# Kernel tuning notes

Hardware: AMD Instinct MI355X
Metric: run time of the kernel (lower is better)

## Reference

```python
import jax, jax.numpy as jnp
import numpy as np

N = 100000   # skill_num
D = 128      # skill_embed_dim
E = 500000   # edges per relation
S = 16384    # queried skills
NEG_SLOPE = 0.2


def _gat(x, edge_index, W, att_src, att_dst, bias):
    # PyG GATConv, heads=1, add_self_loops=True, eval mode (no dropout)
    n = x.shape[0]
    loops = jnp.arange(n)
    src = jnp.concatenate([edge_index[0], loops])
    dst = jnp.concatenate([edge_index[1], loops])
    h = x @ W                              # [N, D]
    a_src = h @ att_src                    # [N]
    a_dst = h @ att_dst                    # [N]
    e = jax.nn.leaky_relu(a_src[src] + a_dst[dst], NEG_SLOPE)  # [E+N]
    emax = jax.ops.segment_max(e, dst, num_segments=n)
    ex = jnp.exp(e - emax[dst])
    denom = jax.ops.segment_sum(ex, dst, num_segments=n)
    alpha = ex / (denom[dst] + 1e-16)
    out = jax.ops.segment_sum(alpha[:, None] * h[src], dst, num_segments=n)
    return out + bias


def _sage(x, edge_index, Wl, bl, Wr):
    # PyG SAGEConv, aggr='mean', root_weight=True (lin_r has no bias)
    n = x.shape[0]
    src, dst = edge_index[0], edge_index[1]
    ones = jnp.ones((src.shape[0],), dtype=x.dtype)
    deg = jax.ops.segment_sum(ones, dst, num_segments=n)
    agg = jax.ops.segment_sum(x[src], dst, num_segments=n)
    agg = agg / jnp.maximum(deg, 1.0)[:, None]
    return agg @ Wl + bl + x @ Wr


def setup_inputs() -> dict:
    key = jax.random.key(0)
    ks = jax.random.split(key, 16)
    sc = 1.0 / np.sqrt(D)
    inp = {
        "s": jax.random.randint(ks[0], (S,), 0, N),
        "t_s": 0,
        "t_e": 12,
        "ei_parent": jax.random.randint(ks[1], (2, E), 0, N),
        "ei_child": jax.random.randint(ks[2], (2, E), 0, N),
        "ei_relate": jax.random.randint(ks[3], (2, E), 0, N),
        "emb": jax.random.normal(ks[4], (N, D), dtype=jnp.float32),
        # GAT is_parent params
        "Wp": jax.random.normal(ks[5], (D, D), dtype=jnp.float32) * sc,
        "asp": jax.random.normal(ks[6], (D,), dtype=jnp.float32) * sc,
        "adp": jax.random.normal(ks[7], (D,), dtype=jnp.float32) * sc,
        "bp": jnp.zeros((D,), dtype=jnp.float32),
        # GAT is_child params
        "Wc": jax.random.normal(ks[8], (D, D), dtype=jnp.float32) * sc,
        "asc": jax.random.normal(ks[9], (D,), dtype=jnp.float32) * sc,
        "adc": jax.random.normal(ks[10], (D,), dtype=jnp.float32) * sc,
        "bc": jnp.zeros((D,), dtype=jnp.float32),
        # SAGE relate params
        "Wl": jax.random.normal(ks[11], (D, D), dtype=jnp.float32) * sc,
        "bl": jnp.zeros((D,), dtype=jnp.float32),
        "Wr": jax.random.normal(ks[12], (D, D), dtype=jnp.float32) * sc,
    }
    return inp


def reference(s, t_s, t_e, ei_parent, ei_child, ei_relate, emb,
              Wp, asp, adp, bp, Wc, asc, adc, bc, Wl, bl, Wr):
    out_parent = _gat(emb, ei_parent, Wp, asp, adp, bp)
    out_child = _gat(emb, ei_child, Wc, asc, adc, bc)
    out_relate = _sage(emb, ei_relate, Wl, bl, Wr)
    # HeteroConv(aggr='mean') over the three relation outputs
    node_out = (out_parent + out_child + out_relate) / 3.0
    return node_out[s, :]
```

## Files before the change

kernel.cpp:

```cpp
#include <hip/hip_runtime.h>

#define D 128
#define CAP 64
#define OVF_CAP 1024

typedef short bf16x8 __attribute__((ext_vector_type(8)));
typedef float f32x4 __attribute__((ext_vector_type(4)));

__device__ __forceinline__ unsigned short f2bf(float f) {
  unsigned u = __builtin_bit_cast(unsigned, f);
  unsigned r = (u + 0x7fffu + ((u >> 16) & 1u)) >> 16;
  return (unsigned short)r;
}
__device__ __forceinline__ float bflo(unsigned r) {
  return __builtin_bit_cast(float, r << 16);
}
__device__ __forceinline__ float bfhi(unsigned r) {
  return __builtin_bit_cast(float, r & 0xffff0000u);
}
__device__ __forceinline__ float lrelu(float t) {
  return t >= 0.f ? t : 0.2f * t;
}
__device__ __forceinline__ int swz(int b) { return b ^ (((b >> 8) & 7) << 4); }


__global__ void k_setup(const float* __restrict__ Wp, const float* __restrict__ asp,
                        const float* __restrict__ adp, const float* __restrict__ Wc,
                        const float* __restrict__ asc, const float* __restrict__ adc,
                        const float* __restrict__ bp, const float* __restrict__ bc,
                        const float* __restrict__ bl, const float* __restrict__ Wl,
                        const float* __restrict__ Wr,
                        float* __restrict__ v, unsigned short* __restrict__ wpack,
                        int* __restrict__ qid, int* __restrict__ counters,
                        int* __restrict__ deg5, int N, int S5) {
  int i = blockIdx.x * blockDim.x + threadIdx.x;
  int stride = gridDim.x * blockDim.x;
  for (int k = i; k < N; k += stride) qid[k] = -1;
  for (int k = i; k < S5; k += stride) deg5[k] = 0;
  if (i < 16) counters[i] = 0;

  for (int idx = i; idx < 16 * 8 * 64 * 8; idx += stride) {
    int j    = idx & 7;
    int lane = (idx >> 3) & 63;
    int nt   = (idx >> 9) & 7;
    int kt   = idx >> 12;
    int o = kt >> 2;
    int c = (kt & 3) * 32 + (lane >> 4) * 8 + j;
    int n = nt * 16 + (lane & 15);
    const float* W = (o == 0) ? Wp : (o == 1) ? Wc : (o == 2) ? Wl : Wr;
    wpack[idx] = f2bf(W[c * D + n]);
  }

  if (blockIdx.x == 0 && threadIdx.x < 128) {
    int k = threadIdx.x;
    float s0 = 0.f, s1 = 0.f, s2 = 0.f, s3 = 0.f;
    for (int d = 0; d < D; ++d) {
      float wp = Wp[k * D + d], wc = Wc[k * D + d];
      s0 += wp * asp[d]; s1 += wp * adp[d];
      s2 += wc * asc[d]; s3 += wc * adc[d];
    }
    v[k] = s0; v[D + k] = s1; v[2 * D + k] = s2; v[3 * D + k] = s3;
    v[4 * D + k] = bp[k] + bc[k] + bl[k];
  }
}

__global__ void k_pre(const int* __restrict__ s, int* __restrict__ qid,
                      int* __restrict__ uniq, int* __restrict__ counters, int S,
                      const float* __restrict__ emb, const float* __restrict__ v,
                      float* __restrict__ a_sp, float* __restrict__ a_dp,
                      float* __restrict__ a_sc, float* __restrict__ a_dc,
                      float* __restrict__ selfP, float* __restrict__ selfC,
                      unsigned* __restrict__ ebf, int N) {
  int gtid = blockIdx.x * blockDim.x + threadIdx.x;
  int lane = threadIdx.x & 63;
  if (gtid < S) {
    int n = s[gtid];
    bool won = (atomicCAS(&qid[n], -1, -2) == -1);
    unsigned long long mask = __ballot(won);
    if (mask != 0ull) {
      int leader = __builtin_ctzll(mask);
      int base = 0;
      if (lane == leader) base = atomicAdd(&counters[0], __popcll(mask));
      base = __shfl(base, leader);
      if (won) {
        int u = base + __popcll(mask & ((1ull << lane) - 1ull));
        uniq[u] = n;
        qid[n] = u;
      }
    }
  }
  int node = (gtid >> 6) * 2 + (lane >> 5);
  int c = lane & 31;
  if (node >= N) return;
  float4 x4 = ((const float4*)(emb + (size_t)node * D))[c];
  uint2 p;
  p.x = ((unsigned)f2bf(x4.x)) | (((unsigned)f2bf(x4.y)) << 16);
  p.y = ((unsigned)f2bf(x4.z)) | (((unsigned)f2bf(x4.w)) << 16);
  ((uint2*)ebf)[(size_t)node * 32 + c] = p;
  float4 v0 = ((const float4*)(v))[c];
  float4 v1 = ((const float4*)(v + D))[c];
  float4 v2 = ((const float4*)(v + 2 * D))[c];
  float4 v3 = ((const float4*)(v + 3 * D))[c];
  float s0 = x4.x * v0.x + x4.y * v0.y + x4.z * v0.z + x4.w * v0.w;
  float s1 = x4.x * v1.x + x4.y * v1.y + x4.z * v1.z + x4.w * v1.w;
  float s2 = x4.x * v2.x + x4.y * v2.y + x4.z * v2.z + x4.w * v2.w;
  float s3 = x4.x * v3.x + x4.y * v3.y + x4.z * v3.z + x4.w * v3.w;
#pragma unroll
  for (int o = 16; o > 0; o >>= 1) {
    s0 += __shfl_down(s0, o);
    s1 += __shfl_down(s1, o);
    s2 += __shfl_down(s2, o);
    s3 += __shfl_down(s3, o);
  }
  if (c == 0) {
    a_sp[node] = s0; a_dp[node] = s1; a_sc[node] = s2; a_dc[node] = s3;
    selfP[node] = __expf(lrelu(s0 + s1));
    selfC[node] = __expf(lrelu(s2 + s3));
  }
}

__global__ void __launch_bounds__(256) k_filter(
    const int* __restrict__ eiP, const int* __restrict__ eiC,
    const int* __restrict__ eiR, const int* __restrict__ qid,
    int2* __restrict__ bktP, int2* __restrict__ bktC, int* __restrict__ bktR,
    int* __restrict__ degP, int* __restrict__ degC, int* __restrict__ degR,
    float* __restrict__ denP, float* __restrict__ denC,
    const float* __restrict__ a_sp, const float* __restrict__ a_dp,
    const float* __restrict__ a_sc, const float* __restrict__ a_dc,
    int2* __restrict__ ovf, int* __restrict__ counters, int E) {
  int rel = blockIdx.y;
  const int* ei = (rel == 0) ? eiP : (rel == 1) ? eiC : eiR;
  int e = blockIdx.x * 256 + threadIdx.x;
  if (e >= E) return;
  int dst = ei[E + e];
  int u = qid[dst];
  if (u < 0) return;
  int src = ei[e];
  int* deg = (rel == 0) ? degP : (rel == 1) ? degC : degR;
  int pos = atomicAdd(&deg[u], 1);
  if (rel == 2) {
    if (pos < CAP) {
      bktR[u * CAP + pos] = src;
    } else {
      int o = atomicAdd(&counters[6], 1);
      if (o < OVF_CAP) { int2 tt; tt.x = src; tt.y = u; ovf[2 * OVF_CAP + o] = tt; }
    }
  } else {
    const float* a_s = (rel == 0) ? a_sp : a_sc;
    const float* a_d = (rel == 0) ? a_dp : a_dc;
    float wgt = __expf(lrelu(a_s[src] + a_d[dst]));
    atomicAdd((rel == 0) ? &denP[u] : &denC[u], wgt);
    if (pos < CAP) {
      int2 tt; tt.x = src; tt.y = __builtin_bit_cast(int, wgt);
      ((rel == 0) ? bktP : bktC)[u * CAP + pos] = tt;
    } else {
      int o = atomicAdd(&counters[4 + rel], 1);
      if (o < OVF_CAP) { int2 tt; tt.x = src; tt.y = u; ovf[rel * OVF_CAP + o] = tt; }
    }
  }
}

__global__ void __launch_bounds__(512, 4) k_fused(
    const int2* __restrict__ bktP, const int2* __restrict__ bktC,
    const int* __restrict__ bktR,
    const int* __restrict__ degP, const int* __restrict__ degC,
    const int* __restrict__ degR,
    const float* __restrict__ denP, const float* __restrict__ denC,
    const float* __restrict__ a_sp, const float* __restrict__ a_dp,
    const float* __restrict__ a_sc, const float* __restrict__ a_dc,
    const float* __restrict__ selfP, const float* __restrict__ selfC,
    const unsigned* __restrict__ ebf, const float* __restrict__ emb,
    const int* __restrict__ uniq, const int* __restrict__ counters,
    const int2* __restrict__ ovf, const float* __restrict__ vvec,
    const unsigned short* __restrict__ wpack, float* __restrict__ outU) {
  __shared__ __align__(16) unsigned short A_lds[16 * 64 * 8];
  int U = counters[0];
  int u0 = blockIdx.x * 16;
  if (u0 >= U) return;
  int tid = threadIdx.x;
  int w = tid >> 6;
  int lane = tid & 63;

  int Lc[3];
#pragma unroll
  for (int r = 0; r < 3; ++r) {
    int L = counters[4 + r];
    Lc[r] = (L > OVF_CAP) ? OVF_CAP : L;
  }

#pragma unroll
  for (int t = 0; t < 2; ++t) {
    int m = 2 * w + t;
    int u = u0 + m;
    float2 z[4];
    if (u < U) {
      int n = uniq[u];
      float2 x2 = ((const float2*)(emb + (size_t)n * D))[lane];
#pragma unroll
      for (int r = 0; r < 3; ++r) {
        int dg = ((r == 0) ? degP : (r == 1) ? degC : degR)[u];
        int mc = (dg < CAP) ? dg : CAP;
        int srcl = 0;
        float wl = 0.f;
        if (r < 2) {
          if (lane < mc) {
            int2 sw_ = ((r == 0) ? bktP : bktC)[u * CAP + lane];
            srcl = sw_.x;
            wl = __builtin_bit_cast(float, sw_.y);
          }
        } else {
          if (lane < mc) { srcl = bktR[u * CAP + lane]; wl = 1.f; }
        }
        float2 a; a.x = 0.f; a.y = 0.f;
        int i = 0;
        for (; i + 4 <= mc; i += 4) {
          int s0 = __shfl(srcl, i),     s1 = __shfl(srcl, i + 1);
          int s2 = __shfl(srcl, i + 2), s3 = __shfl(srcl, i + 3);
          float w0 = __shfl(wl, i),     w1 = __shfl(wl, i + 1);
          float w2 = __shfl(wl, i + 2), w3 = __shfl(wl, i + 3);
          unsigned r0 = ebf[(size_t)s0 * 64 + lane];
          unsigned r1 = ebf[(size_t)s1 * 64 + lane];
          unsigned r2 = ebf[(size_t)s2 * 64 + lane];
          unsigned r3 = ebf[(size_t)s3 * 64 + lane];
          a.x += w0 * bflo(r0) + w1 * bflo(r1) + w2 * bflo(r2) + w3 * bflo(r3);
          a.y += w0 * bfhi(r0) + w1 * bfhi(r1) + w2 * bfhi(r2) + w3 * bfhi(r3);
        }
        for (; i < mc; ++i) {
          int si = __shfl(srcl, i);
          float wi = __shfl(wl, i);
          unsigned rr = ebf[(size_t)si * 64 + lane];
          a.x += wi * bflo(rr);
          a.y += wi * bfhi(rr);
        }
        if (dg > CAP) {
          const float* a_s = (r == 0) ? a_sp : a_sc;
          float adn = (r == 0) ? a_dp[n] : (r == 1) ? a_dc[n] : 0.f;
          for (int l = 0; l < Lc[r]; ++l) {
            int2 ov = ovf[r * OVF_CAP + l];
            if (ov.y == u) {
              float wv = 1.f;
              if (r < 2) wv = __expf(lrelu(a_s[ov.x] + adn));
              unsigned rr = ebf[(size_t)ov.x * 64 + lane];
              a.x += wv * bflo(rr);
              a.y += wv * bfhi(rr);
            }
          }
        }
        if (r == 2) {
          float dgc = (float)dg; if (dgc < 1.f) dgc = 1.f;
          float rc = 1.f / dgc;
          a.x *= rc; a.y *= rc;
        }
        z[r] = a;
      }
      float wP = selfP[n];
      float rP = 1.f / (denP[u] + wP);
      float wC = selfC[n];
      float rC = 1.f / (denC[u] + wC);
      z[0].x = (z[0].x + wP * x2.x) * rP; z[0].y = (z[0].y + wP * x2.y) * rP;
      z[1].x = (z[1].x + wC * x2.x) * rC; z[1].y = (z[1].y + wC * x2.y) * rC;
      z[3] = x2;
    } else {
      z[0].x = 0.f; z[0].y = 0.f; z[1] = z[0]; z[2] = z[0]; z[3] = z[0];
    }
    int ktc = lane >> 4;
    int q = (lane >> 2) & 3;
    int j0 = 2 * (lane & 3);
#pragma unroll
    for (int o = 0; o < 4; ++o) {
      int kt = o * 4 + ktc;
      unsigned pk = ((unsigned)f2bf(z[o].x)) | (((unsigned)f2bf(z[o].y)) << 16);
      int off = ((kt * 64 + q * 16 + m) * 8 + j0) * 2;
      *(unsigned*)((char*)A_lds + swz(off)) = pk;
    }
  }
  __syncthreads();

  f32x4 acc = {0.f, 0.f, 0.f, 0.f};
  const bf16x8* wp = (const bf16x8*)wpack;
#pragma unroll
  for (int kt = 0; kt < 16; ++kt) {
    bf16x8 a = *(const bf16x8*)((const char*)A_lds + swz((kt * 64 + lane) * 16));
    bf16x8 b = wp[(kt * 8 + w) * 64 + lane];
    acc = __builtin_amdgcn_mfma_f32_16x16x32_bf16(a, b, acc, 0, 0, 0);
  }

  int col = w * 16 + (lane & 15);
  int r0 = (lane >> 4) * 4;
  float bv = vvec[4 * D + col] * (1.f / 3.f);
#pragma unroll
  for (int reg = 0; reg < 4; ++reg) {
    int u = u0 + r0 + reg;
    if (u < U) outU[(size_t)u * D + col] = acc[reg] * (1.f / 3.f) + bv;
  }
}

__global__ void k_gather(const int* __restrict__ s, const int* __restrict__ qid,
                         const float* __restrict__ outU, float* __restrict__ out, int S) {
  int idx = blockIdx.x * blockDim.x + threadIdx.x;
  if (idx >= S * D) return;
  int i = idx >> 7;
  int d = idx & (D - 1);
  int u = qid[s[i]];
  out[idx] = outU[(size_t)u * D + d];
}


extern "C" void kernel_launch(void* const* d_in, const int* in_sizes, int n_in,
                              void* d_out, int out_size, void* d_ws, size_t ws_size,
                              hipStream_t stream) {
  const int*   s   = (const int*)d_in[0];
  const int*   eip = (const int*)d_in[3];
  const int*   eic = (const int*)d_in[4];
  const int*   eir = (const int*)d_in[5];
  const float* emb = (const float*)d_in[6];
  const float* Wp  = (const float*)d_in[7];
  const float* asp = (const float*)d_in[8];
  const float* adp = (const float*)d_in[9];
  const float* bp  = (const float*)d_in[10];
  const float* Wc  = (const float*)d_in[11];
  const float* asc = (const float*)d_in[12];
  const float* adc = (const float*)d_in[13];
  const float* bc  = (const float*)d_in[14];
  const float* Wl  = (const float*)d_in[15];
  const float* bl  = (const float*)d_in[16];
  const float* Wr  = (const float*)d_in[17];
  float* out = (float*)d_out;

  const int S = in_sizes[0];
  const int E = in_sizes[3] / 2;
  const int N = in_sizes[6] / D;

  char* base = (char*)d_ws;
  size_t off = 0;
  auto carve = [&](size_t bytes) -> char* {
    char* q = base + off;
    off += (bytes + 255) & ~(size_t)255;
    return q;
  };
  float*    a_sp     = (float*)carve((size_t)N * 4);
  float*    a_dp     = (float*)carve((size_t)N * 4);
  float*    a_sc     = (float*)carve((size_t)N * 4);
  float*    a_dc     = (float*)carve((size_t)N * 4);
  float*    selfP    = (float*)carve((size_t)N * 4);
  float*    selfC    = (float*)carve((size_t)N * 4);
  int*      qid      = (int*)carve((size_t)N * 4);
  unsigned* ebf      = (unsigned*)carve((size_t)N * 64 * 4);
  int*      uniq     = (int*)carve((size_t)S * 4);
  int*      counters = (int*)carve(64);
  float*    vvec     = (float*)carve(5 * D * 4);
  unsigned short* wpack = (unsigned short*)carve((size_t)16 * 8 * 64 * 8 * 2);
  float*    outU     = (float*)carve((size_t)S * D * 4);
  int*      degP     = (int*)carve((size_t)S * 4);
  int*      degC     = (int*)carve((size_t)S * 4);
  int*      degR     = (int*)carve((size_t)S * 4);
  float*    denP     = (float*)carve((size_t)S * 4);
  float*    denC     = (float*)carve((size_t)S * 4);
  int2*     bktP     = (int2*)carve((size_t)S * CAP * 8);
  int2*     bktC     = (int2*)carve((size_t)S * CAP * 8);
  int*      bktR     = (int*)carve((size_t)S * CAP * 4);
  int2*     ovf      = (int2*)carve((size_t)3 * OVF_CAP * 8);
  (void)ws_size; (void)n_in; (void)out_size;

  k_setup<<<256, 256, 0, stream>>>(Wp, asp, adp, Wc, asc, adc, bp, bc, bl, Wl, Wr,
                                   vvec, wpack, qid, counters, degP, N, 5 * S);

  k_pre<<<(N * 32 + 255) / 256, 256, 0, stream>>>(s, qid, uniq, counters, S,
                                                  emb, vvec, a_sp, a_dp, a_sc, a_dc,
                                                  selfP, selfC, ebf, N);

  k_filter<<<dim3((E + 255) / 256, 3), 256, 0, stream>>>(
      eip, eic, eir, qid, bktP, bktC, bktR, degP, degC, degR, denP, denC,
      a_sp, a_dp, a_sc, a_dc, ovf, counters, E);

  k_fused<<<(S + 15) / 16, 512, 0, stream>>>(
      bktP, bktC, bktR, degP, degC, degR, denP, denC,
      a_sp, a_dp, a_sc, a_dc, selfP, selfC, ebf, emb, uniq, counters, ovf,
      vvec, wpack, outU);

  k_gather<<<(S * D + 255) / 256, 256, 0, stream>>>(s, qid, outU, out, S);
}
```

Measured before the change: 195.8 us.

## Parallelize attention-vector setup, vectorize gather, relax fused launch bounds

The W·att projection in k_setup now uses all 256 threads of block 0: each 32-lane group reads float4 rows and reduces them with shuffles, replacing 128 threads that each ran a serial 128-step loop. k_gather now moves float4 per thread, so it issues a quarter as many threads and wider loads and stores. The min-blocks-per-SM hint of 4 is removed from k_fused's launch bounds, which lets the compiler use more registers at the possible cost of occupancy.

```diff
diff --git a/kernel.cpp b/kernel.cpp
--- a/kernel.cpp
+++ b/kernel.cpp
@@ -51,16 +51,35 @@
     wpack[idx] = f2bf(W[c * D + n]);
   }
 
-  if (blockIdx.x == 0 && threadIdx.x < 128) {
-    int k = threadIdx.x;
-    float s0 = 0.f, s1 = 0.f, s2 = 0.f, s3 = 0.f;
-    for (int d = 0; d < D; ++d) {
-      float wp = Wp[k * D + d], wc = Wc[k * D + d];
-      s0 += wp * asp[d]; s1 += wp * adp[d];
-      s2 += wc * asc[d]; s3 += wc * adc[d];
-    }
-    v[k] = s0; v[D + k] = s1; v[2 * D + k] = s2; v[3 * D + k] = s3;
-    v[4 * D + k] = bp[k] + bc[k] + bl[k];
+  if (blockIdx.x == 0) {
+    int hw = threadIdx.x >> 5;
+    int ln = threadIdx.x & 31;
+    float4 as4p = ((const float4*)asp)[ln];
+    float4 ad4p = ((const float4*)adp)[ln];
+    float4 as4c = ((const float4*)asc)[ln];
+    float4 ad4c = ((const float4*)adc)[ln];
+    for (int k = hw; k < D; k += 8) {
+      float4 wp4 = ((const float4*)(Wp + (size_t)k * D))[ln];
+      float4 wc4 = ((const float4*)(Wc + (size_t)k * D))[ln];
+      float s0 = wp4.x * as4p.x + wp4.y * as4p.y + wp4.z * as4p.z + wp4.w * as4p.w;
+      float s1 = wp4.x * ad4p.x + wp4.y * ad4p.y + wp4.z * ad4p.z + wp4.w * ad4p.w;
+      float s2 = wc4.x * as4c.x + wc4.y * as4c.y + wc4.z * as4c.z + wc4.w * as4c.w;
+      float s3 = wc4.x * ad4c.x + wc4.y * ad4c.y + wc4.z * ad4c.z + wc4.w * ad4c.w;
+#pragma unroll
+      for (int o = 16; o > 0; o >>= 1) {
+        s0 += __shfl_down(s0, o, 32);
+        s1 += __shfl_down(s1, o, 32);
+        s2 += __shfl_down(s2, o, 32);
+        s3 += __shfl_down(s3, o, 32);
+      }
+      if (ln == 0) {
+        v[k] = s0; v[D + k] = s1; v[2 * D + k] = s2; v[3 * D + k] = s3;
+      }
+    }
+    if (threadIdx.x < D) {
+      int k = threadIdx.x;
+      v[4 * D + k] = bp[k] + bc[k] + bl[k];
+    }
   }
 }
 
@@ -160,7 +179,7 @@
   }
 }
 
-__global__ void __launch_bounds__(512, 4) k_fused(
+__global__ void __launch_bounds__(512) k_fused(
     const int2* __restrict__ bktP, const int2* __restrict__ bktC,
     const int* __restrict__ bktR,
     const int* __restrict__ degP, const int* __restrict__ degC,
@@ -296,13 +315,14 @@
 }
 
 __global__ void k_gather(const int* __restrict__ s, const int* __restrict__ qid,
-                         const float* __restrict__ outU, float* __restrict__ out, int S) {
+                         const float4* __restrict__ outU4, float4* __restrict__ out4,
+                         int S) {
   int idx = blockIdx.x * blockDim.x + threadIdx.x;
-  if (idx >= S * D) return;
-  int i = idx >> 7;
-  int d = idx & (D - 1);
+  if (idx >= S * 32) return;
+  int i = idx >> 5;
+  int c = idx & 31;
   int u = qid[s[i]];
-  out[idx] = outU[(size_t)u * D + d];
+  out4[idx] = outU4[(size_t)u * 32 + c];
 }
 
 
@@ -378,5 +398,6 @@
       a_sp, a_dp, a_sc, a_dc, selfP, selfC, ebf, emb, uniq, counters, ovf,
       vvec, wpack, outU);
 
-  k_gather<<<(S * D + 255) / 256, 256, 0, stream>>>(s, qid, outU, out, S);
-}
+  k_gather<<<(S * 32 + 255) / 256, 256, 0, stream>>>(s, qid, (const float4*)outU,
+                                                     (float4*)out, S);
+}
```

Result: slower. 202.3 us (+3.3%).
